# Kernel optimization log

Measured on AMD Instinct MI355X. Metric: run time of the kernel, lower is better.

Reference implementation:

```python
import jax, jax.numpy as jnp
import numpy as np

B, T, D_MODEL, HEAD = 8, 2048, 1024, 64
NEG = -1e9  # finite mask fill; exp underflows to 0 in softmax, avoids inf/NaN


def setup_inputs() -> dict:
    key = jax.random.key(0)
    k1, k2, k3, k4, k5 = jax.random.split(key, 5)
    x = jax.random.normal(k1, (B, T, D_MODEL), dtype=jnp.float32)
    valid_lens = jax.random.randint(k2, (B,), 0, T)
    # nn.Linear(d_model, head_size, bias=False): y = x @ W, W: (d_model, head_size)
    s = 0.02
    Wq = jax.random.normal(k3, (D_MODEL, HEAD), dtype=jnp.float32) * s
    Wk = jax.random.normal(k4, (D_MODEL, HEAD), dtype=jnp.float32) * s
    Wv = jax.random.normal(k5, (D_MODEL, HEAD), dtype=jnp.float32) * s
    return {"x": x, "Wq": Wq, "Wk": Wk, "Wv": Wv, "valid_lens": valid_lens}


def reference(x, Wq, Wk, Wv, valid_lens):
    # x: (B, T, D), projections -> (B, T, H)
    q = jnp.einsum("btd,dh->bth", x, Wq)
    k = jnp.einsum("btd,dh->bth", x, Wk)
    v = jnp.einsum("btd,dh->bth", x, Wv)
    scale = k.shape[-1] ** -0.5
    wei = jnp.einsum("bqh,bkh->bqk", q, k) * scale  # (B, T, T)

    t = jnp.arange(T)
    causal = t[None, :] <= t[:, None]                     # (T, T) lower-tri
    valid = t[None, :] < valid_lens[:, None]              # (B, T)
    mask = causal[None, :, :] & valid[:, :, None] & valid[:, None, :]  # (B, T, T)

    wei = jnp.where(mask, wei, NEG)
    attn = jax.nn.softmax(wei, axis=2)
    # rows with no valid key get all-masked scores -> original code zeros them out
    row_all_masked = ~jnp.any(mask, axis=2)               # (B, T)
    attn = jnp.where(row_all_masked[:, :, None], 0.0, attn)
    # dropout(p=0.0) == identity
    out = jnp.einsum("bqk,bkh->bqh", attn, v)             # (B, T, H)
    return out
```

## Files before the change

kernel.cpp:

```cpp
#include <hip/hip_runtime.h>
#include <hip/hip_bf16.h>
#include <stdint.h>

#define T_   2048
#define DM_  1024
#define HD_  64
#define NROW 16384
#define SPLIT 4

typedef __attribute__((ext_vector_type(8))) __bf16 bf16x8;
typedef __attribute__((ext_vector_type(4))) __bf16 bf16x4;
typedef __attribute__((ext_vector_type(4))) float  f32x4;

__global__ void wconv_k(const float* __restrict__ Wq, const float* __restrict__ Wk,
                        const float* __restrict__ Wv, __bf16* __restrict__ wfrag) {
    int tid  = blockIdx.x * 256 + threadIdx.x;
    int lane = tid & 63;
    int t    = (tid >> 6) % 12;
    int kc   = tid / (12 * 64);
    int c = lane & 15, g = lane >> 4;
    int n = t * 16 + c;
    const float* W = (n < 64) ? Wq : (n < 128) ? Wk : Wv;
    int col = n & 63;
    int k0  = kc * 32 + g * 8;
    __bf16* dst = wfrag + (size_t)tid * 8;
#pragma unroll
    for (int j = 0; j < 8; ++j) dst[j] = (__bf16)W[(k0 + j) * HD_ + col];
}

__global__ __launch_bounds__(256) void proj_k(const float* __restrict__ x,
        const __bf16* __restrict__ wfrag, __bf16* __restrict__ Qb,
        __bf16* __restrict__ Kb, __bf16* __restrict__ Vt) {
    int lane = threadIdx.x & 63, wave = threadIdx.x >> 6;
    int ng = blockIdx.x >> 8;
    int rt = blockIdx.x & 255;
    int c = lane & 15, g = lane >> 4;
    int row0 = rt * 64 + wave * 16;
    const float* xp = x + (size_t)(row0 + c) * DM_ + g * 8;
    f32x4 acc[4];
#pragma unroll
    for (int t = 0; t < 4; ++t) acc[t] = (f32x4)0.f;
    for (int kc = 0; kc < 32; ++kc) {
        const f32x4* ap = (const f32x4*)(xp + kc * 32);
        f32x4 a0 = ap[0], a1 = ap[1];
        bf16x8 af;
#pragma unroll
        for (int j = 0; j < 4; ++j) { af[j] = (__bf16)a0[j]; af[j + 4] = (__bf16)a1[j]; }
        const bf16x8* bp = (const bf16x8*)(wfrag + (size_t)kc * 12 * 512) + ng * 256;
#pragma unroll
        for (int t = 0; t < 4; ++t) {
            bf16x8 bf = bp[t * 64 + lane];
            acc[t] = __builtin_amdgcn_mfma_f32_16x16x32_bf16(af, bf, acc[t], 0, 0, 0);
        }
    }
#pragma unroll
    for (int t = 0; t < 4; ++t) {
        int ncol = t * 16 + c;
#pragma unroll
        for (int r = 0; r < 4; ++r) {
            int grow = row0 + g * 4 + r;
            float v  = acc[t][r];
            if (ng == 0)      Qb[(size_t)grow * HD_ + ncol] = (__bf16)(v * 0.18033688f);
            else if (ng == 1) Kb[(size_t)grow * HD_ + ncol] = (__bf16)v;
            else              Vt[(size_t)(grow >> 11) * (HD_ * T_) + (size_t)ncol * T_ + (grow & 2047)] = (__bf16)v;
        }
    }
}

__global__ __launch_bounds__(128) void attn_k(const __bf16* __restrict__ Qb,
        const __bf16* __restrict__ Kb, const __bf16* __restrict__ Vt,
        float* __restrict__ Opart, float* __restrict__ ml) {
    int split = blockIdx.x >> 9;
    int bid2  = blockIdx.x & 511;
    int half = bid2 >> 8, idx = bid2 & 255;
    int b = idx >> 5, p = idx & 31;
    int qb = half ? (63 - p) : p;
    int wave = threadIdx.x >> 6, lane = threadIdx.x & 63;
    int c = lane & 15, g = lane >> 4;
    int qg   = qb * 32 + wave * 16 + c;
    int tile = b * 128 + qb * 2 + wave;
    int nd2  = (qb + 2) >> 1;
    float m = -1e30f, lsum = 0.f;
    if (split < nd2) {
        const __bf16* qp = Qb + (size_t)(b * T_ + qg) * HD_ + g * 8;
        bf16x8 qf0 = *(const bf16x8*)qp;
        bf16x8 qf1 = *(const bf16x8*)(qp + 32);
        const __bf16* Kbase = Kb + (size_t)b * T_ * HD_;
        const __bf16* Vbase = Vt + (size_t)b * HD_ * T_;
        f32x4 o0 = (f32x4)0.f, o1 = (f32x4)0.f, o2 = (f32x4)0.f, o3 = (f32x4)0.f;
        __shared__ __bf16 plds[2][16][72];
        __bf16 (*pl)[72] = plds[wave];
        for (int kt = split; kt < nd2; kt += SPLIT) {
            int kv0 = kt * 64;
            const __bf16* kp = Kbase + (size_t)(kv0 + c) * HD_ + g * 8;
            bf16x8 ka00 = *(const bf16x8*)(kp);
            bf16x8 ka01 = *(const bf16x8*)(kp + 32);
            bf16x8 ka10 = *(const bf16x8*)(kp + 16 * HD_);
            bf16x8 ka11 = *(const bf16x8*)(kp + 16 * HD_ + 32);
            bf16x8 kb00 = *(const bf16x8*)(kp + 32 * HD_);
            bf16x8 kb01 = *(const bf16x8*)(kp + 32 * HD_ + 32);
            bf16x8 kb10 = *(const bf16x8*)(kp + 48 * HD_);
            bf16x8 kb11 = *(const bf16x8*)(kp + 48 * HD_ + 32);
            f32x4 sa0 = (f32x4)0.f, sa1 = (f32x4)0.f, sb0 = (f32x4)0.f, sb1 = (f32x4)0.f;
            sa0 = __builtin_amdgcn_mfma_f32_16x16x32_bf16(ka00, qf0, sa0, 0, 0, 0);
            sa0 = __builtin_amdgcn_mfma_f32_16x16x32_bf16(ka01, qf1, sa0, 0, 0, 0);
            sa1 = __builtin_amdgcn_mfma_f32_16x16x32_bf16(ka10, qf0, sa1, 0, 0, 0);
            sa1 = __builtin_amdgcn_mfma_f32_16x16x32_bf16(ka11, qf1, sa1, 0, 0, 0);
            sb0 = __builtin_amdgcn_mfma_f32_16x16x32_bf16(kb00, qf0, sb0, 0, 0, 0);
            sb0 = __builtin_amdgcn_mfma_f32_16x16x32_bf16(kb01, qf1, sb0, 0, 0, 0);
            sb1 = __builtin_amdgcn_mfma_f32_16x16x32_bf16(kb10, qf0, sb1, 0, 0, 0);
            sb1 = __builtin_amdgcn_mfma_f32_16x16x32_bf16(kb11, qf1, sb1, 0, 0, 0);
            float s[16];
#pragma unroll
            for (int r = 0; r < 4; ++r) {
                s[r] = sa0[r]; s[4 + r] = sa1[r]; s[8 + r] = sb0[r]; s[12 + r] = sb1[r];
            }
            if (kt == nd2 - 1) {
#pragma unroll
                for (int i = 0; i < 16; ++i) {
                    int kv = kv0 + (i >> 2) * 16 + g * 4 + (i & 3);
                    if (kv > qg) s[i] = -1e30f;
                }
            }
            float tm = s[0];
#pragma unroll
            for (int i = 1; i < 16; ++i) tm = fmaxf(tm, s[i]);
            tm = fmaxf(tm, __shfl_xor(tm, 16));
            tm = fmaxf(tm, __shfl_xor(tm, 32));
            float mn = fmaxf(m, tm);
            float al = __builtin_amdgcn_exp2f(m - mn);
            float ps = 0.f;
#pragma unroll
            for (int i = 0; i < 16; ++i) { s[i] = __builtin_amdgcn_exp2f(s[i] - mn); ps += s[i]; }
            ps += __shfl_xor(ps, 16);
            ps += __shfl_xor(ps, 32);
            lsum = lsum * al + ps;
            m = mn;
            o0 *= al; o1 *= al; o2 *= al; o3 *= al;
#pragma unroll
            for (int mt = 0; mt < 4; ++mt) {
                bf16x4 pv;
#pragma unroll
                for (int r = 0; r < 4; ++r) pv[r] = (__bf16)s[mt * 4 + r];
                *(bf16x4*)&pl[c][mt * 16 + g * 4] = pv;
            }
            bf16x8 pf0 = *(const bf16x8*)&pl[c][g * 8];
            bf16x8 pf1 = *(const bf16x8*)&pl[c][32 + g * 8];
            const __bf16* vp = Vbase + (size_t)c * T_ + kv0 + g * 8;
            bf16x8 v0a = *(const bf16x8*)(vp);
            bf16x8 v1a = *(const bf16x8*)(vp + 16 * T_);
            bf16x8 v2a = *(const bf16x8*)(vp + 32 * T_);
            bf16x8 v3a = *(const bf16x8*)(vp + 48 * T_);
            bf16x8 v0b = *(const bf16x8*)(vp + 32);
            bf16x8 v1b = *(const bf16x8*)(vp + 16 * T_ + 32);
            bf16x8 v2b = *(const bf16x8*)(vp + 32 * T_ + 32);
            bf16x8 v3b = *(const bf16x8*)(vp + 48 * T_ + 32);
            o0 = __builtin_amdgcn_mfma_f32_16x16x32_bf16(v0a, pf0, o0, 0, 0, 0);
            o1 = __builtin_amdgcn_mfma_f32_16x16x32_bf16(v1a, pf0, o1, 0, 0, 0);
            o2 = __builtin_amdgcn_mfma_f32_16x16x32_bf16(v2a, pf0, o2, 0, 0, 0);
            o3 = __builtin_amdgcn_mfma_f32_16x16x32_bf16(v3a, pf0, o3, 0, 0, 0);
            o0 = __builtin_amdgcn_mfma_f32_16x16x32_bf16(v0b, pf1, o0, 0, 0, 0);
            o1 = __builtin_amdgcn_mfma_f32_16x16x32_bf16(v1b, pf1, o1, 0, 0, 0);
            o2 = __builtin_amdgcn_mfma_f32_16x16x32_bf16(v2b, pf1, o2, 0, 0, 0);
            o3 = __builtin_amdgcn_mfma_f32_16x16x32_bf16(v3b, pf1, o3, 0, 0, 0);
        }
        float* op = Opart + ((size_t)tile * SPLIT + split) * 1024 + c * 64 + g * 4;
        *(f32x4*)(op)      = o0;
        *(f32x4*)(op + 16) = o1;
        *(f32x4*)(op + 32) = o2;
        *(f32x4*)(op + 48) = o3;
    }
    if (g == 0) {
        float* mlp = ml + ((size_t)tile * SPLIT + split) * 32 + c * 2;
        mlp[0] = m; mlp[1] = lsum;
    }
}

__global__ __launch_bounds__(256) void comb_k(const float* __restrict__ Opart,
        const float* __restrict__ ml, const int* __restrict__ vlen,
        float* __restrict__ out) {
    int tile = blockIdx.x;
    int b  = tile >> 7;
    int q0 = (tile & 127) * 16;
    int q  = threadIdx.x >> 4;
    int d0 = (threadIdx.x & 15) * 4;
    int qg = q0 + q;
    const float* mlp = ml + (size_t)tile * SPLIT * 32 + q * 2;
    float mj[SPLIT], lj[SPLIT];
#pragma unroll
    for (int j = 0; j < SPLIT; ++j) { mj[j] = mlp[j * 32]; lj[j] = mlp[j * 32 + 1]; }
    float M = fmaxf(fmaxf(mj[0], mj[1]), fmaxf(mj[2], mj[3]));
    f32x4 acc = (f32x4)0.f;
    float L = 0.f;
#pragma unroll
    for (int j = 0; j < SPLIT; ++j) {
        if (lj[j] > 0.f) {
            float sc = __builtin_amdgcn_exp2f(mj[j] - M);
            L += lj[j] * sc;
            f32x4 ov = *(const f32x4*)(Opart + ((size_t)tile * SPLIT + j) * 1024 + q * 64 + d0);
            acc += ov * sc;
        }
    }
    float inv = (qg < vlen[b]) ? 1.f / L : 0.f;
    f32x4 r = acc * inv;
    *(f32x4*)(out + ((size_t)(b * T_) + qg) * HD_ + d0) = r;
}

extern "C" void kernel_launch(void* const* d_in, const int* in_sizes, int n_in,
                              void* d_out, int out_size, void* d_ws, size_t ws_size,
                              hipStream_t stream) {
    const float* x   = (const float*)d_in[0];
    const float* Wq  = (const float*)d_in[1];
    const float* Wk  = (const float*)d_in[2];
    const float* Wv  = (const float*)d_in[3];
    const int*   vln = (const int*)d_in[4];
    float* out = (float*)d_out;

    __bf16* Qb    = (__bf16*)d_ws;
    __bf16* Kb    = Qb + (size_t)NROW * HD_;
    __bf16* Vt    = Kb + (size_t)NROW * HD_;
    __bf16* wfrag = Vt + (size_t)NROW * HD_;
    float*  Opart = (float*)(wfrag + 24576 * 8);
    float*  mlbuf = Opart + (size_t)1024 * SPLIT * 1024;

    wconv_k<<<96, 256, 0, stream>>>(Wq, Wk, Wv, wfrag);
    proj_k <<<768, 256, 0, stream>>>(x, wfrag, Qb, Kb, Vt);
    attn_k <<<512 * SPLIT, 128, 0, stream>>>(Qb, Kb, Vt, Opart, mlbuf);
    comb_k <<<1024, 256, 0, stream>>>(Opart, mlbuf, vln, out);
}
```

Baseline: 170.5 us.

## Compute all QKV columns per block with double-buffered LDS staging

The projection kernel is restructured so each block computes all 192 output columns (Q, K and V) for 32 rows, instead of one 64-column group per block. This means x is read once rather than three times. Weight fragments are loaded asynchronously into LDS with global_load_lds, and x tiles are double-buffered in LDS with prefetch of the next k-chunk. The trade-off is more LDS use and barriers per iteration, and fewer blocks (512).

```diff
diff --git a/kernel.cpp b/kernel.cpp
--- a/kernel.cpp
+++ b/kernel.cpp
@@ -7,6 +7,8 @@
 #define HD_  64
 #define NROW 16384
 #define SPLIT 4
+#define BM   32
+#define BK   64
 
 typedef __attribute__((ext_vector_type(8))) __bf16 bf16x8;
 typedef __attribute__((ext_vector_type(4))) __bf16 bf16x4;
@@ -28,41 +30,88 @@
     for (int j = 0; j < 8; ++j) dst[j] = (__bf16)W[(k0 + j) * HD_ + col];
 }
 
-__global__ __launch_bounds__(256) void proj_k(const float* __restrict__ x,
+__global__ __launch_bounds__(256, 2) void proj_k(const float* __restrict__ x,
         const __bf16* __restrict__ wfrag, __bf16* __restrict__ Qb,
         __bf16* __restrict__ Kb, __bf16* __restrict__ Vt) {
-    int lane = threadIdx.x & 63, wave = threadIdx.x >> 6;
-    int ng = blockIdx.x >> 8;
-    int rt = blockIdx.x & 255;
+    __shared__ __bf16 abuf[2][BM][72];
+    __shared__ __bf16 bbuf[2][2][12][512];
+    int tid  = threadIdx.x;
+    int lane = tid & 63, wave = tid >> 6;
+    int mh = wave >> 1, th = wave & 1;
     int c = lane & 15, g = lane >> 4;
-    int row0 = rt * 64 + wave * 16;
-    const float* xp = x + (size_t)(row0 + c) * DM_ + g * 8;
-    f32x4 acc[4];
-#pragma unroll
-    for (int t = 0; t < 4; ++t) acc[t] = (f32x4)0.f;
-    for (int kc = 0; kc < 32; ++kc) {
-        const f32x4* ap = (const f32x4*)(xp + kc * 32);
-        f32x4 a0 = ap[0], a1 = ap[1];
-        bf16x8 af;
-#pragma unroll
-        for (int j = 0; j < 4; ++j) { af[j] = (__bf16)a0[j]; af[j + 4] = (__bf16)a1[j]; }
-        const bf16x8* bp = (const bf16x8*)(wfrag + (size_t)kc * 12 * 512) + ng * 256;
-#pragma unroll
-        for (int t = 0; t < 4; ++t) {
-            bf16x8 bf = bp[t * 64 + lane];
-            acc[t] = __builtin_amdgcn_mfma_f32_16x16x32_bf16(af, bf, acc[t], 0, 0, 0);
-        }
-    }
-#pragma unroll
-    for (int t = 0; t < 4; ++t) {
-        int ncol = t * 16 + c;
+    int row0 = blockIdx.x * BM;
+    int ar = tid >> 3, a0 = (tid & 7) * 8;
+    const float* xrow = x + (size_t)(row0 + ar) * DM_ + a0;
+
+    f32x4 acc[6];
+#pragma unroll
+    for (int t = 0; t < 6; ++t) acc[t] = (f32x4)0.f;
+
+    {
+#pragma unroll
+        for (int i = 0; i < 6; ++i) {
+            int p = wave * 6 + i;
+            int kh = p / 12, tt = p % 12;
+            const __bf16* src = wfrag + ((size_t)kh * 12 + tt) * 512 + lane * 8;
+            __builtin_amdgcn_global_load_lds(
+                (const __attribute__((address_space(1))) void*)src,
+                (__attribute__((address_space(3))) void*)&bbuf[0][kh][tt][0], 16, 0, 0);
+        }
+        f32x4 x0 = *(const f32x4*)(xrow);
+        f32x4 x1 = *(const f32x4*)(xrow + 4);
+        bf16x8 a;
+#pragma unroll
+        for (int j = 0; j < 4; ++j) { a[j] = (__bf16)x0[j]; a[4 + j] = (__bf16)x1[j]; }
+        *(bf16x8*)&abuf[0][ar][a0] = a;
+    }
+
+    for (int kk = 0; kk < 16; ++kk) {
+        int buf = kk & 1, nb = buf ^ 1;
+        __syncthreads();
+        f32x4 x0, x1;
+        bool hn = (kk + 1) < 16;
+        if (hn) {
+            const float* xp = xrow + (kk + 1) * BK;
+            x0 = *(const f32x4*)(xp);
+            x1 = *(const f32x4*)(xp + 4);
+#pragma unroll
+            for (int i = 0; i < 6; ++i) {
+                int p = wave * 6 + i;
+                int kh = p / 12, tt = p % 12;
+                const __bf16* src = wfrag + (((size_t)(kk + 1) * 2 + kh) * 12 + tt) * 512 + lane * 8;
+                __builtin_amdgcn_global_load_lds(
+                    (const __attribute__((address_space(1))) void*)src,
+                    (__attribute__((address_space(3))) void*)&bbuf[nb][kh][tt][0], 16, 0, 0);
+            }
+        }
+#pragma unroll
+        for (int kh = 0; kh < 2; ++kh) {
+            bf16x8 af = *(const bf16x8*)&abuf[buf][mh * 16 + c][kh * 32 + g * 8];
+#pragma unroll
+            for (int t = 0; t < 6; ++t) {
+                bf16x8 bfh = *(const bf16x8*)&bbuf[buf][kh][th * 6 + t][lane * 8];
+                acc[t] = __builtin_amdgcn_mfma_f32_16x16x32_bf16(af, bfh, acc[t], 0, 0, 0);
+            }
+        }
+        if (hn) {
+            bf16x8 a;
+#pragma unroll
+            for (int j = 0; j < 4; ++j) { a[j] = (__bf16)x0[j]; a[4 + j] = (__bf16)x1[j]; }
+            *(bf16x8*)&abuf[nb][ar][a0] = a;
+        }
+    }
+
+#pragma unroll
+    for (int t = 0; t < 6; ++t) {
+        int tg = th * 6 + t;
+        int n  = tg * 16 + c;
 #pragma unroll
         for (int r = 0; r < 4; ++r) {
-            int grow = row0 + g * 4 + r;
+            int grow = row0 + mh * 16 + g * 4 + r;
             float v  = acc[t][r];
-            if (ng == 0)      Qb[(size_t)grow * HD_ + ncol] = (__bf16)(v * 0.18033688f);
-            else if (ng == 1) Kb[(size_t)grow * HD_ + ncol] = (__bf16)v;
-            else              Vt[(size_t)(grow >> 11) * (HD_ * T_) + (size_t)ncol * T_ + (grow & 2047)] = (__bf16)v;
+            if (n < 64)       Qb[(size_t)grow * HD_ + n] = (__bf16)(v * 0.18033688f);
+            else if (n < 128) Kb[(size_t)grow * HD_ + (n - 64)] = (__bf16)v;
+            else              Vt[(size_t)(grow >> 11) * (HD_ * T_) + (size_t)(n - 128) * T_ + (grow & 2047)] = (__bf16)v;
         }
     }
 }
@@ -224,7 +273,7 @@
     float*  mlbuf = Opart + (size_t)1024 * SPLIT * 1024;
 
     wconv_k<<<96, 256, 0, stream>>>(Wq, Wk, Wv, wfrag);
-    proj_k <<<768, 256, 0, stream>>>(x, wfrag, Qb, Kb, Vt);
+    proj_k <<<512, 256, 0, stream>>>(x, wfrag, Qb, Kb, Vt);
     attn_k <<<512 * SPLIT, 128, 0, stream>>>(Qb, Kb, Vt, Opart, mlbuf);
     comb_k <<<1024, 256, 0, stream>>>(Opart, mlbuf, vln, out);
 }
```

After: 155.5 us. -8.8%, faster.
